# Performance work log

Measured on AMD Instinct MI355X. Metric: run time of the kernel, lower is better.

Reference implementation:

```python
import jax, jax.numpy as jnp
import numpy as np

B, C_IN, C_OUT, H, W = 32, 64, 128, 56, 56


def setup_inputs() -> dict:
    key = jax.random.key(0)
    k1, k2, k3 = jax.random.split(key, 3)
    x = jax.random.normal(k1, (B, C_IN, H, W), dtype=jnp.float32)
    # Original build(): kernel ~ N(0,1) in spatial domain, then fft2d; the
    # real/imag parts of the spectrum are the learned variables.
    kernel = jax.random.normal(k2, (C_OUT, C_IN, H, W), dtype=jnp.float32)
    kernel_fft = jnp.fft.fft2(kernel.astype(jnp.complex64))
    kernel_real = jnp.real(kernel_fft).astype(jnp.float32)
    kernel_imag = jnp.imag(kernel_fft).astype(jnp.float32)
    bias = jnp.zeros((C_OUT,), dtype=jnp.float32)
    return {"x": x, "kernel_real": kernel_real, "kernel_imag": kernel_imag, "bias": bias}


def reference(x, kernel_real, kernel_imag, bias):
    # FFT-based convolution, vectorized over batch (original used a per-batch
    # Python loop + concat; math is identical).
    x_fft = jnp.fft.fft2(x.astype(jnp.complex64))              # [B, Cin, H, W]
    kernel_freq = jax.lax.complex(kernel_real, kernel_imag)    # [Cout, Cin, H, W]
    # elementwise complex multiply + reduce over input channels
    y_fft = jnp.einsum('oihw,bihw->bohw', kernel_freq, x_fft)  # [B, Cout, H, W]
    y = jnp.real(jnp.fft.ifft2(y_fft))                         # [B, Cout, H, W]
    return y + bias[None, :, None, None]
```

## Files before the change

### kernel.cpp

```cpp
#include <hip/hip_runtime.h>


#define HH 56
#define NF 3136
#define KH 29
#define NFH 1624
constexpr int B = 32, CIN = 64, COUT = 128;
constexpr float PI2 = 6.283185307179586f;

typedef unsigned short u16;
typedef __attribute__((ext_vector_type(8))) short s8v;
typedef __attribute__((ext_vector_type(4))) float f4v;
typedef __attribute__((ext_vector_type(4))) int i4v;

#define MFMA(a, b, c) __builtin_amdgcn_mfma_f32_16x16x32_bf16(a, b, c, 0, 0, 0)

__device__ __host__ inline short f2bf(float f) {
    unsigned u = __builtin_bit_cast(unsigned, f);
    u += 0x7fffu + ((u >> 16) & 1u);
    return (short)(u >> 16);
}

__device__ inline unsigned pk2(float a, float b) {
    return (unsigned)(u16)f2bf(a) | ((unsigned)(u16)f2bf(b) << 16);
}

__device__ inline s8v negbf(s8v a) {
    i4v t = __builtin_bit_cast(i4v, a);
    t ^= (int)0x80008000u;
    return __builtin_bit_cast(s8v, t);
}

__global__ __launch_bounds__(256) void ksetup(short* __restrict__ cpool) {
    int i = blockIdx.x * 256 + threadIdx.x;
    if (i < 4608) {
        int m = i / 72, n = i % 72;
        float c = 0.f, s = 0.f;
        if (m < 56 && n < 56) {
            float ang = PI2 * (float)((m * n) % 56) / 56.f;
            c = cosf(ang); s = sinf(ang);
        }
        cpool[i]        = f2bf(c);
        cpool[4608 + i] = f2bf(s);
    } else if (i < 7168) {
        int j = i - 4608;
        int h = j / 40, kh = j % 40;
        float c = 0.f, s = 0.f;
        if (h < 56 && kh < 29) {
            float w = (kh == 0 || kh == 28) ? 1.f : 2.f;
            float ang = PI2 * (float)((h * kh) % 56) / 56.f;
            float sc = w * (1.f / 3136.f);
            c = sc * cosf(ang);
            s = -sc * sinf(ang);
        }
        cpool[13824 + j] = f2bf(c);
        cpool[16384 + j] = f2bf(s);
    }
}

__global__ __launch_bounds__(512) void kstage(const float* __restrict__ x,
                                              const float* __restrict__ Kr,
                                              const float* __restrict__ Ki,
                                              const short* __restrict__ cpool,
                                              ushort2* __restrict__ Xb,
                                              u16* __restrict__ Kbr,
                                              u16* __restrict__ Kbi) {
    __shared__ __align__(16) char pool[73728];
    const int tid = threadIdx.x;

    if (blockIdx.x >= 1024) {
        u16* Lr = (u16*)pool;
        u16* Li = Lr + 3840;
        const int t = blockIdx.x - 1024;
        const int oi0 = (t & 127) * 64;
        const int f0  = (t >> 7) * 56;
        for (int c = tid; c < 896; c += 512) {
            int row = c / 14, c4 = (c % 14) * 4;
            size_t g = (size_t)(oi0 + row) * NF + f0 + c4;
            float4 vr = *(const float4*)&Kr[g];
            float4 vi = *(const float4*)&Ki[g];
            *(uint2*)&Lr[row * 60 + c4] = make_uint2(pk2(vr.x, vr.y), pk2(vr.z, vr.w));
            *(uint2*)&Li[row * 60 + c4] = make_uint2(pk2(vi.x, vi.y), pk2(vi.z, vi.w));
        }
        __syncthreads();
        for (int idx = tid; idx < 896; idx += 512) {
            int c = idx & 15, f = idx >> 4;
            int j0 = c * 4;
            unsigned r01 = (unsigned)Lr[j0 * 60 + f]       | ((unsigned)Lr[(j0 + 1) * 60 + f] << 16);
            unsigned r23 = (unsigned)Lr[(j0 + 2) * 60 + f] | ((unsigned)Lr[(j0 + 3) * 60 + f] << 16);
            unsigned i01 = (unsigned)Li[j0 * 60 + f]       | ((unsigned)Li[(j0 + 1) * 60 + f] << 16);
            unsigned i23 = (unsigned)Li[(j0 + 2) * 60 + f] | ((unsigned)Li[(j0 + 3) * 60 + f] << 16);
            size_t o = (size_t)(f0 + f) * 8192 + oi0 + j0;
            *(uint2*)&Kbr[o] = make_uint2(r01, r23);
            *(uint2*)&Kbi[o] = make_uint2(i01, i23);
        }
        return;
    }

    short* Cw  = (short*)pool;
    short* Sw  = Cw + 4608;
    short* xs  = Sw + 4608;
    short* T1r = xs + 9216;
    short* T1i = T1r + 9216;
    {
        const int4* src = (const int4*)cpool;
        for (int i = tid; i < 576; i += 512) {
            ((int4*)Cw)[i] = src[i];
            ((int4*)Sw)[i] = src[576 + i];
        }
    }
    for (int i = tid; i < 4608; i += 512) ((int*)xs)[i] = 0;
    __syncthreads();
    const int half = tid >> 8, tid2 = tid & 255;
    const float* xp = x + (size_t)(blockIdx.x * 2 + half) * NF;
    short* xsh = xs + half * 4608;
    for (int c = tid2; c < 784; c += 256) {
        int r = c / 14, c4 = (c % 14) * 4;
        float4 v = *(const float4*)&xp[r * 56 + c4];
        *(uint2*)&xsh[r * 72 + c4] = make_uint2(pk2(v.x, v.y), pk2(v.z, v.w));
    }
    __syncthreads();

    const int lane = tid & 63;
    const int wv = tid >> 6;
    const int hw = wv >> 2;
    const int nt = wv & 3;
    const int q = lane >> 4, l15 = lane & 15;

    f4v aR[4] = {}, aI[4] = {};
    for (int ks = 0; ks < 2; ++ks) {
        const int bo = (nt * 16 + l15) * 72 + ks * 32 + q * 8;
        s8v bC  = *(const s8v*)&Cw[bo];
        s8v bSN = negbf(*(const s8v*)&Sw[bo]);
        for (int mt = 0; mt < 4; ++mt) {
            s8v a = *(const s8v*)&xs[hw * 4608 + (mt * 16 + l15) * 72 + ks * 32 + q * 8];
            aR[mt] = MFMA(a, bC, aR[mt]);
            aI[mt] = MFMA(a, bSN, aI[mt]);
        }
    }
    for (int mt = 0; mt < 4; ++mt) {
        int o = hw * 4608 + (nt * 16 + l15) * 72 + mt * 16 + q * 4;
        *(uint2*)&T1r[o] = make_uint2(pk2(aR[mt][0], aR[mt][1]),
                                      pk2(aR[mt][2], aR[mt][3]));
        *(uint2*)&T1i[o] = make_uint2(pk2(aI[mt][0], aI[mt][1]),
                                      pk2(aI[mt][2], aI[mt][3]));
    }
    __syncthreads();

    f4v xr[2] = {}, xi2[2] = {};
    for (int ks = 0; ks < 2; ++ks) {
        const int bo = hw * 4608 + (nt * 16 + l15) * 72 + ks * 32 + q * 8;
        s8v br = *(const s8v*)&T1r[bo];
        s8v bi = *(const s8v*)&T1i[bo];
        for (int mt = 0; mt < 2; ++mt) {
            const int ao = (mt * 16 + l15) * 72 + ks * 32 + q * 8;
            s8v aC  = *(const s8v*)&Cw[ao];
            s8v aS  = *(const s8v*)&Sw[ao];
            s8v aSN = negbf(aS);
            xr[mt]  = MFMA(aC, br, xr[mt]);
            xr[mt]  = MFMA(aS, bi, xr[mt]);
            xi2[mt] = MFMA(aC, bi, xi2[mt]);
            xi2[mt] = MFMA(aSN, br, xi2[mt]);
        }
    }
    ushort2* op = Xb + (size_t)(blockIdx.x * 2 + hw) * NFH;
    const int kw = nt * 16 + l15;
    if (kw < 56) {
        for (int mt = 0; mt < 2; ++mt)
            for (int r = 0; r < 4; ++r) {
                int kh = mt * 16 + q * 4 + r;
                if (kh < 29)
                    op[kh * 56 + kw] = make_ushort2((u16)f2bf(xr[mt][r]),
                                                    (u16)f2bf(xi2[mt][r]));
            }
    }
}

__global__ __launch_bounds__(256) void kmix(const ushort2* __restrict__ Xb,
                                            const u16* __restrict__ Kbr,
                                            const u16* __restrict__ Kbi,
                                            ushort2* __restrict__ Yb) {
    __shared__ __align__(16) u16 Xr[8 * 2304], Xi[8 * 2304];
    const int tid = threadIdx.x;
    const int f0 = blockIdx.x * 8;
    const int o0 = blockIdx.y * 64;

    for (int rr = 0; rr < 8; ++rr) {
        int row = rr * 256 + tid;
        const uint4* src = (const uint4*)(Xb + (size_t)row * NFH + f0);
        uint4 v0 = src[0], v1 = src[1];
        int base = (row >> 6) * 72 + (row & 63);
        unsigned uu[8] = {v0.x, v0.y, v0.z, v0.w, v1.x, v1.y, v1.z, v1.w};
        #pragma unroll
        for (int ff = 0; ff < 8; ++ff) {
            Xr[ff * 2304 + base] = (u16)uu[ff];
            Xi[ff * 2304 + base] = (u16)(uu[ff] >> 16);
        }
    }
    __syncthreads();

    const int lane = tid & 63;
    const int wv = tid >> 6;
    const int q = lane >> 4, l15 = lane & 15;
    const int o = o0 + wv * 16 + l15;

    unsigned pk[2][4][8];

    #pragma unroll
    for (int ff = 0; ff < 8; ++ff) {
        const int f = f0 + ff;
        const size_t kb = (size_t)f * 8192 + (size_t)o * 64 + q * 8;
        s8v bkr0 = *(const s8v*)&Kbr[kb];
        s8v bkr1 = *(const s8v*)&Kbr[kb + 32];
        s8v bki0 = *(const s8v*)&Kbi[kb];
        s8v bki1 = *(const s8v*)&Kbi[kb + 32];

        f4v yr[2] = {}, yi[2] = {};
        #pragma unroll
        for (int mt = 0; mt < 2; ++mt) {
            const int ao = ff * 2304 + (mt * 16 + l15) * 72 + q * 8;
            s8v axr0 = *(const s8v*)&Xr[ao];
            s8v axr1 = *(const s8v*)&Xr[ao + 32];
            s8v axi0 = *(const s8v*)&Xi[ao];
            s8v axi1 = *(const s8v*)&Xi[ao + 32];
            s8v axn0 = negbf(axi0), axn1 = negbf(axi1);
            yr[mt] = MFMA(axr0, bkr0, yr[mt]);
            yr[mt] = MFMA(axn0, bki0, yr[mt]);
            yr[mt] = MFMA(axr1, bkr1, yr[mt]);
            yr[mt] = MFMA(axn1, bki1, yr[mt]);
            yi[mt] = MFMA(axr0, bki0, yi[mt]);
            yi[mt] = MFMA(axi0, bkr0, yi[mt]);
            yi[mt] = MFMA(axr1, bki1, yi[mt]);
            yi[mt] = MFMA(axi1, bkr1, yi[mt]);
        }
        #pragma unroll
        for (int mt = 0; mt < 2; ++mt)
            #pragma unroll
            for (int r = 0; r < 4; ++r)
                pk[mt][r][ff] = (unsigned)(u16)f2bf(yr[mt][r]) |
                                ((unsigned)(u16)f2bf(yi[mt][r]) << 16);
    }

    #pragma unroll
    for (int mt = 0; mt < 2; ++mt)
        #pragma unroll
        for (int r = 0; r < 4; ++r) {
            const int b = mt * 16 + q * 4 + r;
            uint4* dst = (uint4*)(Yb + (size_t)(b * COUT + o) * NFH + f0);
            dst[0] = make_uint4(pk[mt][r][0], pk[mt][r][1],
                                pk[mt][r][2], pk[mt][r][3]);
            dst[1] = make_uint4(pk[mt][r][4], pk[mt][r][5],
                                pk[mt][r][6], pk[mt][r][7]);
        }
}

__global__ __launch_bounds__(512) void kinv(const ushort2* __restrict__ Yf,
                                            const short* __restrict__ cpool,
                                            const float* __restrict__ bias,
                                            float* __restrict__ out) {
    __shared__ __align__(16) char pool[49152];
    short* Cw    = (short*)pool;
    short* Sw    = Cw + 4608;
    short* A2C   = Sw + 4608;
    short* A2S   = A2C + 2560;
    short* Ybase = A2S + 2560;
    short* Yr    = Ybase;
    short* Yi    = Yr + 4608;
    short* ZTr   = Ybase;
    short* ZTi   = ZTr + 5120;
    const int tid = threadIdx.x;
    {
        const int4* src = (const int4*)cpool;
        for (int i = tid; i < 576; i += 512) {
            ((int4*)Cw)[i] = src[i];
            ((int4*)Sw)[i] = src[576 + i];
        }
        for (int i = tid; i < 320; i += 512) {
            ((int4*)A2C)[i] = src[1728 + i];
            ((int4*)A2S)[i] = src[2048 + i];
        }
    }
    for (int i = tid; i < 4608; i += 512) ((int*)Ybase)[i] = 0;
    __syncthreads();
    const int half = tid >> 8, tid2 = tid & 255;
    const ushort2* yp = Yf + (size_t)(blockIdx.x * 2 + half) * NFH;
    short* Yrh = Yr + half * 2304;
    short* Yih = Yi + half * 2304;
    for (int c = tid2; c < 406; c += 256) {
        uint4 v = *(const uint4*)&yp[c * 4];
        int f = c * 4, kh = f / 56, kwb = f % 56;
        int o = kh * 72 + kwb;
        *(uint2*)&Yrh[o] = make_uint2((v.x & 0xffffu) | (v.y << 16),
                                      (v.z & 0xffffu) | (v.w << 16));
        *(uint2*)&Yih[o] = make_uint2((v.x >> 16) | (v.y & 0xffff0000u),
                                      (v.z >> 16) | (v.w & 0xffff0000u));
    }
    __syncthreads();

    const int lane = tid & 63;
    const int wv = tid >> 6;
    const int hw = wv >> 2, nt = wv & 3;
    const int q = lane >> 4, l15 = lane & 15;

    f4v zr[2] = {}, zi[2] = {};
    for (int ks = 0; ks < 2; ++ks) {
        const int bo = (nt * 16 + l15) * 72 + ks * 32 + q * 8;
        s8v bC = *(const s8v*)&Cw[bo];
        s8v bS = *(const s8v*)&Sw[bo];
        for (int mt = 0; mt < 2; ++mt) {
            const int ao = hw * 2304 + (mt * 16 + l15) * 72 + ks * 32 + q * 8;
            s8v ar  = *(const s8v*)&Yr[ao];
            s8v ai  = *(const s8v*)&Yi[ao];
            s8v ain = negbf(ai);
            zr[mt] = MFMA(ar, bC, zr[mt]);
            zr[mt] = MFMA(ain, bS, zr[mt]);
            zi[mt] = MFMA(ar, bS, zi[mt]);
            zi[mt] = MFMA(ai, bC, zi[mt]);
        }
    }
    __syncthreads();
    for (int mt = 0; mt < 2; ++mt) {
        int o = hw * 2560 + (nt * 16 + l15) * 40 + mt * 16 + q * 4;
        *(uint2*)&ZTr[o] = make_uint2(pk2(zr[mt][0], zr[mt][1]),
                                      pk2(zr[mt][2], zr[mt][3]));
        *(uint2*)&ZTi[o] = make_uint2(pk2(zi[mt][0], zi[mt][1]),
                                      pk2(zi[mt][2], zi[mt][3]));
    }
    __syncthreads();

    f4v yv[4] = {};
    {
        const int bo = hw * 2560 + (nt * 16 + l15) * 40 + q * 8;
        s8v br = *(const s8v*)&ZTr[bo];
        s8v bi = *(const s8v*)&ZTi[bo];
        for (int mt = 0; mt < 4; ++mt) {
            const int ao = (mt * 16 + l15) * 40 + q * 8;
            s8v ac  = *(const s8v*)&A2C[ao];
            s8v as_ = *(const s8v*)&A2S[ao];
            yv[mt] = MFMA(ac, br, yv[mt]);
            yv[mt] = MFMA(as_, bi, yv[mt]);
        }
    }
    const int img = blockIdx.x * 2 + hw;
    const float bv = bias[img & (COUT - 1)];
    float* opx = out + (size_t)img * NF;
    const int w = nt * 16 + l15;
    if (w < 56) {
        for (int mt = 0; mt < 4; ++mt)
            for (int r = 0; r < 4; ++r) {
                int h = mt * 16 + q * 4 + r;
                if (h < 56) opx[h * 56 + w] = yv[mt][r] + bv;
            }
    }
}

extern "C" void kernel_launch(void* const* d_in, const int* in_sizes, int n_in,
                              void* d_out, int out_size, void* d_ws, size_t ws_size,
                              hipStream_t stream) {
    const float* x    = (const float*)d_in[0];
    const float* Kr   = (const float*)d_in[1];
    const float* Ki   = (const float*)d_in[2];
    const float* bias = (const float*)d_in[3];

    short*   cpool = (short*)d_ws;
    ushort2* Xb  = (ushort2*)((char*)d_ws + 40960);
    ushort2* Yb  = (ushort2*)((char*)d_ws + 40960 + 13307904);
    u16*     Kbr = (u16*)((char*)d_ws + 40960 + 13307904 + 26615808);
    u16*     Kbi = Kbr + (size_t)13307904;

    hipLaunchKernelGGL(ksetup, dim3(28), dim3(256), 0, stream, cpool);
    hipLaunchKernelGGL(kstage, dim3(1024 + 3712), dim3(512), 0, stream,
                       x, Kr, Ki, cpool, Xb, Kbr, Kbi);
    hipLaunchKernelGGL(kmix, dim3(NFH / 8, 2), dim3(256), 0, stream,
                       Xb, Kbr, Kbi, Yb);
    hipLaunchKernelGGL(kinv, dim3(B * COUT / 2), dim3(512), 0, stream,
                       Yb, cpool, bias, (float*)d_out);
}
```

Measured before the change: 302.8 us.

## Fuse kernel-spectrum bf16 conversion into channel-mix kernel with swizzled LDS tiles

Drops the separate pass that converted and transposed the fp32 kernel spectrum into bf16 workspace arrays. The mix kernel now reads the fp32 kernel values directly for its 8-frequency tile, converts them to bf16 and stages them in XOR-swizzled shared memory alongside the input spectrum. It also regrids the mix kernel to 512 threads over 32 output channels with waves split by frequency, batch and output tile. This removes one full write and read of the large kernel tensor, at the cost of 128KB of LDS per block, which limits occupancy to one block per CU.

```diff
diff --git a/kernel.cpp b/kernel.cpp
--- a/kernel.cpp
+++ b/kernel.cpp
@@ -58,50 +58,13 @@
     }
 }
 
-__global__ __launch_bounds__(512) void kstage(const float* __restrict__ x,
-                                              const float* __restrict__ Kr,
-                                              const float* __restrict__ Ki,
-                                              const short* __restrict__ cpool,
-                                              ushort2* __restrict__ Xb,
-                                              u16* __restrict__ Kbr,
-                                              u16* __restrict__ Kbi) {
-    __shared__ __align__(16) char pool[73728];
+__global__ __launch_bounds__(512) void kfwd(const float* __restrict__ x,
+                                            const short* __restrict__ cpool,
+                                            ushort2* __restrict__ Xb) {
+    __shared__ __align__(16) short Cw[4608], Sw[4608];
+    __shared__ __align__(16) short xs[2][4608];
+    __shared__ __align__(16) short T1r[2][4608], T1i[2][4608];
     const int tid = threadIdx.x;
-
-    if (blockIdx.x >= 1024) {
-        u16* Lr = (u16*)pool;
-        u16* Li = Lr + 3840;
-        const int t = blockIdx.x - 1024;
-        const int oi0 = (t & 127) * 64;
-        const int f0  = (t >> 7) * 56;
-        for (int c = tid; c < 896; c += 512) {
-            int row = c / 14, c4 = (c % 14) * 4;
-            size_t g = (size_t)(oi0 + row) * NF + f0 + c4;
-            float4 vr = *(const float4*)&Kr[g];
-            float4 vi = *(const float4*)&Ki[g];
-            *(uint2*)&Lr[row * 60 + c4] = make_uint2(pk2(vr.x, vr.y), pk2(vr.z, vr.w));
-            *(uint2*)&Li[row * 60 + c4] = make_uint2(pk2(vi.x, vi.y), pk2(vi.z, vi.w));
-        }
-        __syncthreads();
-        for (int idx = tid; idx < 896; idx += 512) {
-            int c = idx & 15, f = idx >> 4;
-            int j0 = c * 4;
-            unsigned r01 = (unsigned)Lr[j0 * 60 + f]       | ((unsigned)Lr[(j0 + 1) * 60 + f] << 16);
-            unsigned r23 = (unsigned)Lr[(j0 + 2) * 60 + f] | ((unsigned)Lr[(j0 + 3) * 60 + f] << 16);
-            unsigned i01 = (unsigned)Li[j0 * 60 + f]       | ((unsigned)Li[(j0 + 1) * 60 + f] << 16);
-            unsigned i23 = (unsigned)Li[(j0 + 2) * 60 + f] | ((unsigned)Li[(j0 + 3) * 60 + f] << 16);
-            size_t o = (size_t)(f0 + f) * 8192 + oi0 + j0;
-            *(uint2*)&Kbr[o] = make_uint2(r01, r23);
-            *(uint2*)&Kbi[o] = make_uint2(i01, i23);
-        }
-        return;
-    }
-
-    short* Cw  = (short*)pool;
-    short* Sw  = Cw + 4608;
-    short* xs  = Sw + 4608;
-    short* T1r = xs + 9216;
-    short* T1i = T1r + 9216;
     {
         const int4* src = (const int4*)cpool;
         for (int i = tid; i < 576; i += 512) {
@@ -113,7 +76,7 @@
     __syncthreads();
     const int half = tid >> 8, tid2 = tid & 255;
     const float* xp = x + (size_t)(blockIdx.x * 2 + half) * NF;
-    short* xsh = xs + half * 4608;
+    short* xsh = xs[half];
     for (int c = tid2; c < 784; c += 256) {
         int r = c / 14, c4 = (c % 14) * 4;
         float4 v = *(const float4*)&xp[r * 56 + c4];
@@ -133,25 +96,25 @@
         s8v bC  = *(const s8v*)&Cw[bo];
         s8v bSN = negbf(*(const s8v*)&Sw[bo]);
         for (int mt = 0; mt < 4; ++mt) {
-            s8v a = *(const s8v*)&xs[hw * 4608 + (mt * 16 + l15) * 72 + ks * 32 + q * 8];
+            s8v a = *(const s8v*)&xs[hw][(mt * 16 + l15) * 72 + ks * 32 + q * 8];
             aR[mt] = MFMA(a, bC, aR[mt]);
             aI[mt] = MFMA(a, bSN, aI[mt]);
         }
     }
     for (int mt = 0; mt < 4; ++mt) {
-        int o = hw * 4608 + (nt * 16 + l15) * 72 + mt * 16 + q * 4;
-        *(uint2*)&T1r[o] = make_uint2(pk2(aR[mt][0], aR[mt][1]),
-                                      pk2(aR[mt][2], aR[mt][3]));
-        *(uint2*)&T1i[o] = make_uint2(pk2(aI[mt][0], aI[mt][1]),
-                                      pk2(aI[mt][2], aI[mt][3]));
+        int o = (nt * 16 + l15) * 72 + mt * 16 + q * 4;
+        *(uint2*)&T1r[hw][o] = make_uint2(pk2(aR[mt][0], aR[mt][1]),
+                                          pk2(aR[mt][2], aR[mt][3]));
+        *(uint2*)&T1i[hw][o] = make_uint2(pk2(aI[mt][0], aI[mt][1]),
+                                          pk2(aI[mt][2], aI[mt][3]));
     }
     __syncthreads();
 
     f4v xr[2] = {}, xi2[2] = {};
     for (int ks = 0; ks < 2; ++ks) {
-        const int bo = hw * 4608 + (nt * 16 + l15) * 72 + ks * 32 + q * 8;
-        s8v br = *(const s8v*)&T1r[bo];
-        s8v bi = *(const s8v*)&T1i[bo];
+        const int bo = (nt * 16 + l15) * 72 + ks * 32 + q * 8;
+        s8v br = *(const s8v*)&T1r[hw][bo];
+        s8v bi = *(const s8v*)&T1i[hw][bo];
         for (int mt = 0; mt < 2; ++mt) {
             const int ao = (mt * 16 + l15) * 72 + ks * 32 + q * 8;
             s8v aC  = *(const s8v*)&Cw[ao];
@@ -176,82 +139,101 @@
     }
 }
 
-__global__ __launch_bounds__(256) void kmix(const ushort2* __restrict__ Xb,
-                                            const u16* __restrict__ Kbr,
-                                            const u16* __restrict__ Kbi,
+__global__ __launch_bounds__(512) void kmix(const ushort2* __restrict__ Xb,
+                                            const float* __restrict__ Kr,
+                                            const float* __restrict__ Ki,
                                             ushort2* __restrict__ Yb) {
-    __shared__ __align__(16) u16 Xr[8 * 2304], Xi[8 * 2304];
+    __shared__ __align__(16) char pool[131072];
     const int tid = threadIdx.x;
     const int f0 = blockIdx.x * 8;
-    const int o0 = blockIdx.y * 64;
-
-    for (int rr = 0; rr < 8; ++rr) {
-        int row = rr * 256 + tid;
+    const int o0 = blockIdx.y * 32;
+
+    for (int it = 0; it < 4; ++it) {
+        int row = it * 512 + tid;
         const uint4* src = (const uint4*)(Xb + (size_t)row * NFH + f0);
         uint4 v0 = src[0], v1 = src[1];
-        int base = (row >> 6) * 72 + (row & 63);
+        int b = row >> 6, i = row & 63;
+        int sw = (b * 128 + i * 2) ^ ((b & 7) << 4);
         unsigned uu[8] = {v0.x, v0.y, v0.z, v0.w, v1.x, v1.y, v1.z, v1.w};
         #pragma unroll
         for (int ff = 0; ff < 8; ++ff) {
-            Xr[ff * 2304 + base] = (u16)uu[ff];
-            Xi[ff * 2304 + base] = (u16)(uu[ff] >> 16);
+            *(u16*)(pool + ff * 4096 + sw)         = (u16)uu[ff];
+            *(u16*)(pool + 32768 + ff * 4096 + sw) = (u16)(uu[ff] >> 16);
+        }
+    }
+    for (int it = 0; it < 4; ++it) {
+        int r = it * 512 + tid;
+        int ol = r >> 6, i = r & 63;
+        size_t g = ((size_t)((o0 + ol) * CIN + i)) * NF + f0;
+        int sw = (ol * 128 + i * 2) ^ ((ol & 7) << 4);
+        {
+            float4 a = *(const float4*)&Kr[g];
+            float4 c = *(const float4*)&Kr[g + 4];
+            float vv[8] = {a.x, a.y, a.z, a.w, c.x, c.y, c.z, c.w};
+            #pragma unroll
+            for (int ff = 0; ff < 8; ++ff)
+                *(u16*)(pool + 65536 + ff * 4096 + sw) = (u16)f2bf(vv[ff]);
+        }
+        {
+            float4 a = *(const float4*)&Ki[g];
+            float4 c = *(const float4*)&Ki[g + 4];
+            float vv[8] = {a.x, a.y, a.z, a.w, c.x, c.y, c.z, c.w};
+            #pragma unroll
+            for (int ff = 0; ff < 8; ++ff)
+                *(u16*)(pool + 98304 + ff * 4096 + sw) = (u16)f2bf(vv[ff]);
         }
     }
     __syncthreads();
 
     const int lane = tid & 63;
     const int wv = tid >> 6;
+    const int ffh = wv >> 2, bh = (wv >> 1) & 1, ot = wv & 1;
     const int q = lane >> 4, l15 = lane & 15;
-    const int o = o0 + wv * 16 + l15;
-
-    unsigned pk[2][4][8];
+
+    const int bb = bh * 16 + l15;
+    const int oo = ot * 16 + l15;
+    const int xa0 = (bb * 128 + q * 16)      ^ ((bb & 7) << 4);
+    const int xa1 = (bb * 128 + q * 16 + 64) ^ ((bb & 7) << 4);
+    const int ka0 = (oo * 128 + q * 16)      ^ ((oo & 7) << 4);
+    const int ka1 = (oo * 128 + q * 16 + 64) ^ ((oo & 7) << 4);
+
+    unsigned pk[4][4];
 
     #pragma unroll
-    for (int ff = 0; ff < 8; ++ff) {
-        const int f = f0 + ff;
-        const size_t kb = (size_t)f * 8192 + (size_t)o * 64 + q * 8;
-        s8v bkr0 = *(const s8v*)&Kbr[kb];
-        s8v bkr1 = *(const s8v*)&Kbr[kb + 32];
-        s8v bki0 = *(const s8v*)&Kbi[kb];
-        s8v bki1 = *(const s8v*)&Kbi[kb + 32];
-
-        f4v yr[2] = {}, yi[2] = {};
+    for (int ffc = 0; ffc < 4; ++ffc) {
+        const int fb = (ffh * 4 + ffc) * 4096;
+        s8v axr0 = *(const s8v*)(pool + fb + xa0);
+        s8v axr1 = *(const s8v*)(pool + fb + xa1);
+        s8v axi0 = *(const s8v*)(pool + 32768 + fb + xa0);
+        s8v axi1 = *(const s8v*)(pool + 32768 + fb + xa1);
+        s8v bkr0 = *(const s8v*)(pool + 65536 + fb + ka0);
+        s8v bkr1 = *(const s8v*)(pool + 65536 + fb + ka1);
+        s8v bki0 = *(const s8v*)(pool + 98304 + fb + ka0);
+        s8v bki1 = *(const s8v*)(pool + 98304 + fb + ka1);
+        s8v axn0 = negbf(axi0), axn1 = negbf(axi1);
+        f4v yr = {}, yi = {};
+        yr = MFMA(axr0, bkr0, yr);
+        yr = MFMA(axn0, bki0, yr);
+        yr = MFMA(axr1, bkr1, yr);
+        yr = MFMA(axn1, bki1, yr);
+        yi = MFMA(axr0, bki0, yi);
+        yi = MFMA(axi0, bkr0, yi);
+        yi = MFMA(axr1, bki1, yi);
+        yi = MFMA(axi1, bkr1, yi);
         #pragma unroll
-        for (int mt = 0; mt < 2; ++mt) {
-            const int ao = ff * 2304 + (mt * 16 + l15) * 72 + q * 8;
-            s8v axr0 = *(const s8v*)&Xr[ao];
-            s8v axr1 = *(const s8v*)&Xr[ao + 32];
-            s8v axi0 = *(const s8v*)&Xi[ao];
-            s8v axi1 = *(const s8v*)&Xi[ao + 32];
-            s8v axn0 = negbf(axi0), axn1 = negbf(axi1);
-            yr[mt] = MFMA(axr0, bkr0, yr[mt]);
-            yr[mt] = MFMA(axn0, bki0, yr[mt]);
-            yr[mt] = MFMA(axr1, bkr1, yr[mt]);
-            yr[mt] = MFMA(axn1, bki1, yr[mt]);
-            yi[mt] = MFMA(axr0, bki0, yi[mt]);
-            yi[mt] = MFMA(axi0, bkr0, yi[mt]);
-            yi[mt] = MFMA(axr1, bki1, yi[mt]);
-            yi[mt] = MFMA(axi1, bkr1, yi[mt]);
-        }
-        #pragma unroll
-        for (int mt = 0; mt < 2; ++mt)
-            #pragma unroll
-            for (int r = 0; r < 4; ++r)
-                pk[mt][r][ff] = (unsigned)(u16)f2bf(yr[mt][r]) |
-                                ((unsigned)(u16)f2bf(yi[mt][r]) << 16);
-    }
-
+        for (int r = 0; r < 4; ++r)
+            pk[r][ffc] = (unsigned)(u16)f2bf(yr[r]) |
+                         ((unsigned)(u16)f2bf(yi[r]) << 16);
+    }
+
+    const int o_out = o0 + oo;
     #pragma unroll
-    for (int mt = 0; mt < 2; ++mt)
-        #pragma unroll
-        for (int r = 0; r < 4; ++r) {
-            const int b = mt * 16 + q * 4 + r;
-            uint4* dst = (uint4*)(Yb + (size_t)(b * COUT + o) * NFH + f0);
-            dst[0] = make_uint4(pk[mt][r][0], pk[mt][r][1],
-                                pk[mt][r][2], pk[mt][r][3]);
-            dst[1] = make_uint4(pk[mt][r][4], pk[mt][r][5],
-                                pk[mt][r][6], pk[mt][r][7]);
-        }
+    for (int r = 0; r < 4; ++r) {
+        const int b_out = bh * 16 + q * 4 + r;
+        uint4* dst = (uint4*)(Yb + (size_t)(b_out * COUT + o_out) * NFH
+                              + f0 + ffh * 4);
+        *dst = make_uint4(pk[r][0], pk[r][1], pk[r][2], pk[r][3]);
+    }
 }
 
 __global__ __launch_bounds__(512) void kinv(const ushort2* __restrict__ Yf,
@@ -363,16 +345,14 @@
     const float* bias = (const float*)d_in[3];
 
     short*   cpool = (short*)d_ws;
-    ushort2* Xb  = (ushort2*)((char*)d_ws + 40960);
-    ushort2* Yb  = (ushort2*)((char*)d_ws + 40960 + 13307904);
-    u16*     Kbr = (u16*)((char*)d_ws + 40960 + 13307904 + 26615808);
-    u16*     Kbi = Kbr + (size_t)13307904;
+    ushort2* Xb = (ushort2*)((char*)d_ws + 40960);
+    ushort2* Yb = (ushort2*)((char*)d_ws + 40960 + 13307904);
 
     hipLaunchKernelGGL(ksetup, dim3(28), dim3(256), 0, stream, cpool);
-    hipLaunchKernelGGL(kstage, dim3(1024 + 3712), dim3(512), 0, stream,
-                       x, Kr, Ki, cpool, Xb, Kbr, Kbi);
-    hipLaunchKernelGGL(kmix, dim3(NFH / 8, 2), dim3(256), 0, stream,
-                       Xb, Kbr, Kbi, Yb);
+    hipLaunchKernelGGL(kfwd, dim3(B * CIN / 2), dim3(512), 0, stream,
+                       x, cpool, Xb);
+    hipLaunchKernelGGL(kmix, dim3(NFH / 8, 4), dim3(512), 0, stream,
+                       Xb, Kr, Ki, Yb);
     hipLaunchKernelGGL(kinv, dim3(B * COUT / 2), dim3(512), 0, stream,
                        Yb, cpool, bias, (float*)d_out);
 }
```

New measurement: 330.6 us. 9.2% more time.
